# Kernel tuning notes

Measured on AMD Instinct MI355X. Metric: run time of the kernel, lower is better.

The kernel has to match this reference:

```python
import jax, jax.numpy as jnp
import numpy as np

N_TOKENS, DIM = 4096, 2048
N_EXPERTS, TOPK, INTER = 32, 4, 1408
ALPHA, LIMIT, LIN_OFFSET = 1.702, 7.0, 1.0


def quick_geglu(h, probs):
    # h: [..., 2*INTER], interleaved gate/up as in the torch code (x[..., ::2], x[..., 1::2])
    gate = jnp.minimum(h[..., ::2], LIMIT)
    up = jnp.clip(h[..., 1::2], -LIMIT, LIMIT)
    glu = gate * jax.nn.sigmoid(ALPHA * gate)
    return glu * (up + LIN_OFFSET) * probs


def setup_inputs() -> dict:
    key = jax.random.key(0)
    k1, k2, k3, k4, k5 = jax.random.split(key, 5)
    x = jax.random.normal(k1, (N_TOKENS, DIM), dtype=jnp.float32)
    token_mask = jnp.ones((N_TOKENS,), dtype=bool)
    w = jax.random.uniform(k2, (N_TOKENS, TOPK), dtype=jnp.float32)
    weights = w / jnp.sum(w, axis=-1, keepdims=True)  # routing probs
    indices = jax.random.randint(k3, (N_TOKENS, TOPK), 0, N_EXPERTS, dtype=jnp.int64)
    gate_and_up_projs = 0.02 * jax.random.normal(k4, (N_EXPERTS, DIM, 2 * INTER), dtype=jnp.float32)
    down_projs = 0.02 * jax.random.normal(k5, (N_EXPERTS, INTER, DIM), dtype=jnp.float32)
    return {"x": x, "token_mask": token_mask, "weights": weights, "indices": indices,
            "gate_and_up_projs": gate_and_up_projs, "down_projs": down_projs}


def _moe_forward(x, weights, gup, down, token_mask, indices):
    N, D = x.shape
    E = gup.shape[0]
    topk = indices.shape[1]
    T = N * topk
    C = 2 * ((T + E - 1) // E)

    # masked tokens get expert id -1 (as in _permute_tokens_for_grouped_mm)
    flat_e = jnp.where(token_mask[:, None], indices, -1).reshape(-1)
    valid = flat_e >= 0
    e_id = jnp.where(valid, flat_e, E).astype(jnp.int32)  # invalid -> overflow group E
    w = jnp.where(valid, weights.reshape(-1).astype(jnp.float32), 0.0)
    tok = jnp.repeat(jnp.arange(N, dtype=jnp.int32), topk)

    # stable sort by expert (permutation step)
    order = jnp.argsort(e_id)
    se, st, sw = e_id[order], tok[order], w[order]

    # rank of each sorted assignment within its expert group
    counts = jnp.bincount(e_id, length=E + 1)
    starts = jnp.concatenate([jnp.zeros((1,), jnp.int32), jnp.cumsum(counts).astype(jnp.int32)])
    rank = jnp.arange(T, dtype=jnp.int32) - starts[se]
    valid_slot = (se < E) & (rank < C)
    dest = jnp.where(valid_slot, se * C + rank, E * C)  # overflow/dump row E*C

    # scatter permuted tokens into padded per-expert buffers [E, C, D]
    xb = jnp.zeros((E * C + 1, D), x.dtype).at[dest].set(x[st])
    pb = jnp.zeros((E * C + 1,), jnp.float32).at[dest].set(sw)
    tb = jnp.full((E * C + 1,), N, jnp.int32).at[dest].set(st)

    xg = xb[:E * C].reshape(E, C, D)
    h = jnp.einsum('ecd,edh->ech', xg, gup)                       # grouped gate+up GEMM
    a = quick_geglu(h, pb[:E * C].reshape(E, C, 1)).astype(x.dtype)  # fused act * probs
    y = jnp.einsum('ech,ehd->ecd', a, down).reshape(E * C, D)      # grouped down GEMM

    # combine: scatter-add back to token positions (empty slots have prob 0 -> y == 0)
    out = jnp.zeros((N + 1, D), x.dtype).at[tb[:E * C]].add(y)
    return out[:N]


def reference(x, token_mask, weights, indices, gate_and_up_projs, down_projs):
    return _moe_forward(x, weights, gate_and_up_projs, down_projs, token_mask, indices)
```

## Files before the change

kernel.cpp:

```cpp
#include <hip/hip_runtime.h>
#include <hip/hip_bf16.h>
#include <cstdint>
#include <cstddef>

#define N_TOKENS  4096
#define DIM       2048
#define N_EXPERTS 32
#define TOPK      4
#define INTER     1408
#define TWO_INTER 2816
#define CAP       1024
#define T_ASSIGN  (N_TOKENS*TOPK)
#define BK        32

typedef __attribute__((ext_vector_type(8))) short short8;
typedef __attribute__((ext_vector_type(4))) float f32x4;

__device__ __forceinline__ unsigned pack_bf16(float a, float b) {
  unsigned ua = __builtin_bit_cast(unsigned, a);
  unsigned ub = __builtin_bit_cast(unsigned, b);
  ua = (ua + 0x8000u) >> 16;
  ub = (ub + 0x8000u) & 0xFFFF0000u;
  return ua | ub;
}
__device__ __forceinline__ unsigned short bf16_1(float a) {
  return (unsigned short)((__builtin_bit_cast(unsigned, a) + 0x8000u) >> 16);
}
__device__ __forceinline__ float bf2f(unsigned u16) {
  return __builtin_bit_cast(float, u16 << 16);
}

__device__ __forceinline__ void gl_lds16(const void* g, void* l) {
  __builtin_amdgcn_global_load_lds(
      (const __attribute__((address_space(1))) unsigned int*)g,
      (__attribute__((address_space(3))) unsigned int*)l, 16, 0, 0);
}

__global__ void k_build(const int* __restrict__ tmask, const float* __restrict__ w,
                        const int* __restrict__ idx, int* __restrict__ counts,
                        int* __restrict__ tok, float* __restrict__ pb,
                        int* __restrict__ pos) {
  int i = blockIdx.x * 256 + threadIdx.x;
  if (i >= T_ASSIGN) return;
  int t = i >> 2;
  int e = idx[i];
  if (e < 0 || e >= N_EXPERTS) return;
  if (tmask[t] == 0) return;
  int r = atomicAdd(&counts[e], 1);
  if (r < CAP) {
    tok[e * CAP + r] = t;
    pb[e * CAP + r] = w[i];
    pos[i] = e * CAP + r;
  }
}

__global__ __launch_bounds__(256) void k_conv(const float* __restrict__ src,
                                              __hip_bfloat16* __restrict__ dst, int n4) {
  int i = blockIdx.x * 256 + threadIdx.x;
  int stride = gridDim.x * 256;
  for (; i < n4; i += stride) {
    float4 v = *(const float4*)(src + (size_t)i * 4);
    *(uint2*)(dst + (size_t)i * 4) = make_uint2(pack_bf16(v.x, v.y), pack_bf16(v.z, v.w));
  }
}

__global__ __launch_bounds__(256) void k_tconv(const float* __restrict__ src,
                                               __hip_bfloat16* __restrict__ dst,
                                               int R, int C) {
  __shared__ unsigned short s[64][88];
  int nrt = R >> 6, nct = C >> 6;
  int bid = blockIdx.x;
  int e  = bid / (nrt * nct);
  int rr = bid % (nrt * nct);
  int rt = rr / nct, ct = rr % nct;
  int r0 = rt * 64, c0 = ct * 64;
  const float* sp = src + (size_t)e * R * C;
  int t = threadIdx.x;
  int lr  = t >> 4;
  int lc4 = (t & 15) * 4;
  #pragma unroll
  for (int p = 0; p < 4; ++p) {
    int r = lr + p * 16;
    float4 v = *(const float4*)(sp + (size_t)(r0 + r) * C + c0 + lc4);
    s[lc4 + 0][r] = bf16_1(v.x);
    s[lc4 + 1][r] = bf16_1(v.y);
    s[lc4 + 2][r] = bf16_1(v.z);
    s[lc4 + 3][r] = bf16_1(v.w);
  }
  __syncthreads();
  __hip_bfloat16* dp = dst + (size_t)e * C * R;
  int wc   = t >> 2;
  int wr16 = (t & 3) * 16;
  uint4 o0 = *(const uint4*)&s[wc][wr16];
  uint4 o1 = *(const uint4*)&s[wc][wr16 + 8];
  __hip_bfloat16* o = dp + (size_t)(c0 + wc) * R + r0 + wr16;
  *(uint4*)o = o0;
  *(uint4*)(o + 8) = o1;
}

__global__ __launch_bounds__(256) void k_combine(const __hip_bfloat16* __restrict__ y,
                                                 const int* __restrict__ pos,
                                                 float* __restrict__ out) {
  int gid = blockIdx.x * 256 + threadIdx.x;
  int t  = gid >> 8;
  int c8 = (gid & 255) * 8;
  int4 p = *(const int4*)(pos + t * 4);
  float s[8] = {0.f, 0.f, 0.f, 0.f, 0.f, 0.f, 0.f, 0.f};
  #pragma unroll
  for (int k = 0; k < 4; ++k) {
    int pp = (k == 0) ? p.x : (k == 1) ? p.y : (k == 2) ? p.z : p.w;
    if (pp >= 0) {
      uint4 v = *(const uint4*)(y + (size_t)pp * DIM + c8);
      s[0] += bf2f(v.x & 0xffffu); s[1] += bf2f(v.x >> 16);
      s[2] += bf2f(v.y & 0xffffu); s[3] += bf2f(v.y >> 16);
      s[4] += bf2f(v.z & 0xffffu); s[5] += bf2f(v.z >> 16);
      s[6] += bf2f(v.w & 0xffffu); s[7] += bf2f(v.w >> 16);
    }
  }
  float* o = out + (size_t)t * DIM + c8;
  *(float4*)o       = make_float4(s[0], s[1], s[2], s[3]);
  *(float4*)(o + 4) = make_float4(s[4], s[5], s[6], s[7]);
}


#define STGX(tt, KT) do {                                              \
    if ((tt) < (KT)) {                                                 \
      const int k0_ = (tt) * BK;                                       \
      char* base_ = smem + ((tt) & 1) * 24576;                         \
      gl_lds16(aR0 + k0_, base_ + w * 2048 + lane * 16);               \
      gl_lds16(aR1 + k0_, base_ + w * 2048 + 1024 + lane * 16);        \
      gl_lds16(bR  + k0_, base_ + 16384 + w * 1024 + lane * 16);       \
    }                                                                  \
  } while (0)

#define KLOOP(KT) do {                                                 \
    STGX(0, KT);                                                       \
    _Pragma("unroll 1")                                                \
    for (int t = 0; t < (KT); ++t) {                                   \
      STGX(t + 1, KT);                                                 \
      if (t + 1 < (KT)) { asm volatile("s_waitcnt vmcnt(3)" ::: "memory"); } \
      else             { asm volatile("s_waitcnt vmcnt(0)" ::: "memory"); } \
      __builtin_amdgcn_s_barrier();                                    \
      const char* Ab_ = smem + (t & 1) * 24576;                        \
      const char* Bb_ = Ab_ + 16384;                                   \
      short8 af_[4], bf_[4];                                           \
      _Pragma("unroll")                                                \
      for (int mi_ = 0; mi_ < 4; ++mi_)                                \
        af_[mi_] = *(const short8*)(Ab_ + (wr * 64 + mi_ * 16 + (lane & 15)) * 64 + rch); \
      _Pragma("unroll")                                                \
      for (int ni_ = 0; ni_ < 4; ++ni_)                                \
        bf_[ni_] = *(const short8*)(Bb_ + (wc * 64 + ni_ * 16 + (lane & 15)) * 64 + rch); \
      __builtin_amdgcn_s_setprio(1);                                   \
      _Pragma("unroll")                                                \
      for (int mi_ = 0; mi_ < 4; ++mi_)                                \
        _Pragma("unroll")                                              \
        for (int ni_ = 0; ni_ < 4; ++ni_)                              \
          acc[mi_][ni_] = __builtin_amdgcn_mfma_f32_16x16x32_bf16(     \
              af_[mi_], bf_[ni_], acc[mi_][ni_], 0, 0, 0);             \
      __builtin_amdgcn_s_setprio(0);                                   \
      __builtin_amdgcn_s_barrier();                                    \
    }                                                                  \
  } while (0)

__global__ __launch_bounds__(512, 4) void k_gemm1p(
    const __hip_bfloat16* __restrict__ xb, const __hip_bfloat16* __restrict__ gupT,
    const int* __restrict__ counts, const int* __restrict__ tok,
    const float* __restrict__ pb, __hip_bfloat16* __restrict__ act)
{
  __shared__ char smem[49152];
  const int NT = TWO_INTER / 128;
  const int KT = DIM / BK;
  const int xcd  = blockIdx.x & 7;
  const int slot = blockIdx.x >> 3;
  const int tid = threadIdx.x, lane = tid & 63, w = tid >> 6;
  const int wr = w >> 1, wc = w & 1;
  const int csw = ((lane & 3) ^ ((lane >> 3) & 3)) * 8;
  const int rch = (((lane >> 4) ^ ((lane >> 1) & 3)) << 4);
  const int rA0 = w * 32 + (lane >> 2);
  const int rB  = w * 16 + (lane >> 2);

  int k = 0;
  for (int ei = 0; ei < 4; ++ei) {
    const int e = xcd * 4 + ei;
    int cc = counts[e]; cc = cc > CAP ? CAP : cc;
    const int mtc = (cc + 255) >> 8;
    for (int nt = 0; nt < NT; ++nt)
      for (int mt = 0; mt < mtc; ++mt, ++k) {
        if ((k & 63) != slot) continue;
        const int m0 = mt * 256, n0 = nt * 128;
        __syncthreads();

        const __hip_bfloat16* gT = gupT + (size_t)e * TWO_INTER * DIM;
        const __hip_bfloat16* aR0 = xb + (size_t)tok[e * CAP + m0 + rA0] * DIM + csw;
        const __hip_bfloat16* aR1 = xb + (size_t)tok[e * CAP + m0 + rA0 + 16] * DIM + csw;
        const __hip_bfloat16* bR  = gT + (size_t)(n0 + rB) * DIM + csw;

        f32x4 acc[4][4];
        #pragma unroll
        for (int i = 0; i < 4; ++i)
          #pragma unroll
          for (int j = 0; j < 4; ++j) acc[i][j] = (f32x4){0.f, 0.f, 0.f, 0.f};

        KLOOP(KT);

        const int colp = lane & 15;
        const int rgrp = lane >> 4;
        #pragma unroll
        for (int mi = 0; mi < 4; ++mi) {
          #pragma unroll
          for (int j = 0; j < 4; ++j) {
            int rowl = wr * 64 + mi * 16 + rgrp * 4 + j;
            float prob = pb[e * CAP + m0 + rowl];
            size_t arow = (size_t)(e * CAP + m0 + rowl) * INTER;
            #pragma unroll
            for (int ni = 0; ni < 4; ++ni) {
              float v = acc[mi][ni][j];
              float other = __shfl_xor(v, 1, 64);
              if ((lane & 1) == 0) {
                float gate = fminf(v, 7.0f);
                float up   = fminf(fmaxf(other, -7.0f), 7.0f);
                float glu  = gate / (1.0f + __expf(-1.702f * gate));
                float a    = glu * (up + 1.0f) * prob;
                int nh = n0 + wc * 64 + ni * 16 + colp;
                act[arow + (nh >> 1)] = __float2bfloat16(a);
              }
            }
          }
        }
      }
  }
}

__global__ __launch_bounds__(512, 4) void k_gemm2p(
    const __hip_bfloat16* __restrict__ act, const __hip_bfloat16* __restrict__ downT,
    const int* __restrict__ counts, __hip_bfloat16* __restrict__ y)
{
  __shared__ char smem[49152];
  const int NT = DIM / 128;
  const int KT = INTER / BK;
  const int xcd  = blockIdx.x & 7;
  const int slot = blockIdx.x >> 3;
  const int tid = threadIdx.x, lane = tid & 63, w = tid >> 6;
  const int wr = w >> 1, wc = w & 1;
  const int csw = ((lane & 3) ^ ((lane >> 3) & 3)) * 8;
  const int rch = (((lane >> 4) ^ ((lane >> 1) & 3)) << 4);
  const int rA0 = w * 32 + (lane >> 2);
  const int rB  = w * 16 + (lane >> 2);

  int k = 0;
  for (int ei = 0; ei < 4; ++ei) {
    const int e = xcd * 4 + ei;
    int cc = counts[e]; cc = cc > CAP ? CAP : cc;
    const int mtc = (cc + 255) >> 8;
    for (int nt = 0; nt < NT; ++nt)
      for (int mt = 0; mt < mtc; ++mt, ++k) {
        if ((k & 63) != slot) continue;
        const int m0 = mt * 256, n0 = nt * 128;
        __syncthreads();

        const __hip_bfloat16* dT = downT + (size_t)e * DIM * INTER;
        const __hip_bfloat16* aR0 = act + (size_t)(e * CAP + m0 + rA0) * INTER + csw;
        const __hip_bfloat16* aR1 = act + (size_t)(e * CAP + m0 + rA0 + 16) * INTER + csw;
        const __hip_bfloat16* bR  = dT + (size_t)(n0 + rB) * INTER + csw;

        f32x4 acc[4][4];
        #pragma unroll
        for (int i = 0; i < 4; ++i)
          #pragma unroll
          for (int j = 0; j < 4; ++j) acc[i][j] = (f32x4){0.f, 0.f, 0.f, 0.f};

        KLOOP(KT);

        const int colp = lane & 15;
        const int rgrp = lane >> 4;
        #pragma unroll
        for (int mi = 0; mi < 4; ++mi) {
          #pragma unroll
          for (int j = 0; j < 4; ++j) {
            int rowl = wr * 64 + mi * 16 + rgrp * 4 + j;
            __hip_bfloat16* yrow = y + (size_t)(e * CAP + m0 + rowl) * DIM + n0;
            #pragma unroll
            for (int ni = 0; ni < 4; ++ni)
              yrow[wc * 64 + ni * 16 + colp] = __float2bfloat16(acc[mi][ni][j]);
          }
        }
      }
  }
}


extern "C" void kernel_launch(void* const* d_in, const int* in_sizes, int n_in,
                              void* d_out, int out_size, void* d_ws, size_t ws_size,
                              hipStream_t stream) {
  const float* x     = (const float*)d_in[0];
  const int*   tmask = (const int*)d_in[1];
  const float* w     = (const float*)d_in[2];
  const int*   idx   = (const int*)d_in[3];
  const float* gup   = (const float*)d_in[4];
  const float* down  = (const float*)d_in[5];
  float* out = (float*)d_out;

  char* ws = (char*)d_ws;
  const size_t off_tok   = 256;
  const size_t off_pb    = off_tok + 131072;
  const size_t off_pos   = off_pb + 131072;
  const size_t off_act   = off_pos + 65536;
  const size_t act_bytes = (size_t)N_EXPERTS * CAP * INTER * 2;
  const size_t off_xb    = off_act + act_bytes;
  const size_t xb_bytes  = (size_t)N_TOKENS * DIM * 2;
  const size_t off_gupT  = off_xb + xb_bytes;
  const size_t gupT_b    = (size_t)N_EXPERTS * TWO_INTER * DIM * 2;
  const size_t off_downT = off_gupT + gupT_b;

  int*   counts = (int*)ws;
  int*   tok    = (int*)(ws + off_tok);
  float* pbuf   = (float*)(ws + off_pb);
  int*   pos    = (int*)(ws + off_pos);
  __hip_bfloat16* act   = (__hip_bfloat16*)(ws + off_act);
  __hip_bfloat16* xb    = (__hip_bfloat16*)(ws + off_xb);
  __hip_bfloat16* gupT  = (__hip_bfloat16*)(ws + off_gupT);
  __hip_bfloat16* downT = (__hip_bfloat16*)(ws + off_downT);
  __hip_bfloat16* y     = (__hip_bfloat16*)(ws + off_gupT);

  hipMemsetAsync(ws, 0, off_pos, stream);
  hipMemsetAsync(ws + off_pos, 0xFF, 65536, stream);
  k_build<<<(T_ASSIGN + 255) / 256, 256, 0, stream>>>(tmask, w, idx, counts, tok, pbuf, pos);

  k_conv<<<2048, 256, 0, stream>>>(x, xb, (N_TOKENS * DIM) / 4);
  k_tconv<<<N_EXPERTS * (DIM / 64) * (TWO_INTER / 64), 256, 0, stream>>>(gup, gupT, DIM, TWO_INTER);
  k_tconv<<<N_EXPERTS * (INTER / 64) * (DIM / 64), 256, 0, stream>>>(down, downT, INTER, DIM);

  k_gemm1p<<<512, 512, 0, stream>>>(xb, gupT, counts, tok, pbuf, act);
  k_gemm2p<<<512, 512, 0, stream>>>(act, downT, counts, y);
  k_combine<<<N_TOKENS, 256, 0, stream>>>(y, pos, out);
}
```

Measured before the change: 878.5 us.

## Read fp32 weights directly in GEMMs and use atomic work queues per XCD

Drops the two transpose-and-convert kernels that turned the expert weights into bf16 transposed copies. The GEMMs now load fp32 weight tiles straight into a larger LDS buffer and convert them to bf16 while building the MFMA B fragments, using strided scalar LDS reads. Static round-robin tile assignment is replaced by a per-XCD atomic counter work queue. This avoids a full extra read and write of the weights, but doubles the B bytes loaded per tile, adds LDS read and conversion ALU work in the inner loop, and raises LDS use per block.

```diff
diff --git a/kernel.cpp b/kernel.cpp
--- a/kernel.cpp
+++ b/kernel.cpp
@@ -62,40 +62,6 @@
     float4 v = *(const float4*)(src + (size_t)i * 4);
     *(uint2*)(dst + (size_t)i * 4) = make_uint2(pack_bf16(v.x, v.y), pack_bf16(v.z, v.w));
   }
-}
-
-__global__ __launch_bounds__(256) void k_tconv(const float* __restrict__ src,
-                                               __hip_bfloat16* __restrict__ dst,
-                                               int R, int C) {
-  __shared__ unsigned short s[64][88];
-  int nrt = R >> 6, nct = C >> 6;
-  int bid = blockIdx.x;
-  int e  = bid / (nrt * nct);
-  int rr = bid % (nrt * nct);
-  int rt = rr / nct, ct = rr % nct;
-  int r0 = rt * 64, c0 = ct * 64;
-  const float* sp = src + (size_t)e * R * C;
-  int t = threadIdx.x;
-  int lr  = t >> 4;
-  int lc4 = (t & 15) * 4;
-  #pragma unroll
-  for (int p = 0; p < 4; ++p) {
-    int r = lr + p * 16;
-    float4 v = *(const float4*)(sp + (size_t)(r0 + r) * C + c0 + lc4);
-    s[lc4 + 0][r] = bf16_1(v.x);
-    s[lc4 + 1][r] = bf16_1(v.y);
-    s[lc4 + 2][r] = bf16_1(v.z);
-    s[lc4 + 3][r] = bf16_1(v.w);
-  }
-  __syncthreads();
-  __hip_bfloat16* dp = dst + (size_t)e * C * R;
-  int wc   = t >> 2;
-  int wr16 = (t & 3) * 16;
-  uint4 o0 = *(const uint4*)&s[wc][wr16];
-  uint4 o1 = *(const uint4*)&s[wc][wr16 + 8];
-  __hip_bfloat16* o = dp + (size_t)(c0 + wc) * R + r0 + wr16;
-  *(uint4*)o = o0;
-  *(uint4*)(o + 8) = o1;
 }
 
 __global__ __launch_bounds__(256) void k_combine(const __hip_bfloat16* __restrict__ y,
@@ -123,168 +89,204 @@
 }
 
 
-#define STGX(tt, KT) do {                                              \
-    if ((tt) < (KT)) {                                                 \
-      const int k0_ = (tt) * BK;                                       \
-      char* base_ = smem + ((tt) & 1) * 24576;                         \
-      gl_lds16(aR0 + k0_, base_ + w * 2048 + lane * 16);               \
-      gl_lds16(aR1 + k0_, base_ + w * 2048 + 1024 + lane * 16);        \
-      gl_lds16(bR  + k0_, base_ + 16384 + w * 1024 + lane * 16);       \
-    }                                                                  \
+#define STG(tt, KT) do {                                                     \
+    if ((tt) < (KT)) {                                                       \
+      char* base_ = smem + ((tt) & 1) * 32768;                               \
+      const int ka_ = (tt) * BK;                                             \
+      gl_lds16(aR0 + ka_, base_ + w * 2048 + lane * 16);                     \
+      gl_lds16(aR1 + ka_, base_ + w * 2048 + 1024 + lane * 16);              \
+      const size_t kb_ = (size_t)(tt) * BK * LDB;                            \
+      gl_lds16(bR0 + kb_, base_ + 16384 + w * 1024 + lane * 16);             \
+      gl_lds16(bR1 + kb_, base_ + 16384 + 8192 + w * 1024 + lane * 16);      \
+    }                                                                        \
   } while (0)
 
-#define KLOOP(KT) do {                                                 \
-    STGX(0, KT);                                                       \
-    _Pragma("unroll 1")                                                \
-    for (int t = 0; t < (KT); ++t) {                                   \
-      STGX(t + 1, KT);                                                 \
-      if (t + 1 < (KT)) { asm volatile("s_waitcnt vmcnt(3)" ::: "memory"); } \
-      else             { asm volatile("s_waitcnt vmcnt(0)" ::: "memory"); } \
-      __builtin_amdgcn_s_barrier();                                    \
-      const char* Ab_ = smem + (t & 1) * 24576;                        \
-      const char* Bb_ = Ab_ + 16384;                                   \
-      short8 af_[4], bf_[4];                                           \
-      _Pragma("unroll")                                                \
-      for (int mi_ = 0; mi_ < 4; ++mi_)                                \
+#define KLOOP(KT) do {                                                       \
+    STG(0, KT);                                                              \
+    _Pragma("unroll 1")                                                      \
+    for (int t = 0; t < (KT); ++t) {                                         \
+      STG(t + 1, KT);                                                        \
+      if (t + 1 < (KT)) { asm volatile("s_waitcnt vmcnt(4)" ::: "memory"); } \
+      else             { asm volatile("s_waitcnt vmcnt(0)" ::: "memory"); }  \
+      __builtin_amdgcn_s_barrier();                                          \
+      const char* Ab_ = smem + (t & 1) * 32768;                              \
+      const float* bq_ = (const float*)(Ab_ + 16384 + ((lane >> 4) << 3) * 512) \
+                         + (wc * 64 + (lane & 15));                          \
+      short8 af_[4];                                                         \
+      _Pragma("unroll")                                                      \
+      for (int mi_ = 0; mi_ < 4; ++mi_)                                      \
         af_[mi_] = *(const short8*)(Ab_ + (wr * 64 + mi_ * 16 + (lane & 15)) * 64 + rch); \
-      _Pragma("unroll")                                                \
-      for (int ni_ = 0; ni_ < 4; ++ni_)                                \
-        bf_[ni_] = *(const short8*)(Bb_ + (wc * 64 + ni_ * 16 + (lane & 15)) * 64 + rch); \
-      __builtin_amdgcn_s_setprio(1);                                   \
-      _Pragma("unroll")                                                \
-      for (int mi_ = 0; mi_ < 4; ++mi_)                                \
-        _Pragma("unroll")                                              \
-        for (int ni_ = 0; ni_ < 4; ++ni_)                              \
-          acc[mi_][ni_] = __builtin_amdgcn_mfma_f32_16x16x32_bf16(     \
-              af_[mi_], bf_[ni_], acc[mi_][ni_], 0, 0, 0);             \
-      __builtin_amdgcn_s_setprio(0);                                   \
-      __builtin_amdgcn_s_barrier();                                    \
-    }                                                                  \
+      _Pragma("unroll")                                                      \
+      for (int ni_ = 0; ni_ < 4; ++ni_) {                                    \
+        const float* q_ = bq_ + ni_ * 16;                                    \
+        short8 bf_;                                                          \
+        _Pragma("unroll")                                                    \
+        for (int j_ = 0; j_ < 8; ++j_)                                       \
+          bf_[j_] = (short)bf16_1(q_[j_ * 128]);                             \
+        __builtin_amdgcn_s_setprio(1);                                       \
+        _Pragma("unroll")                                                    \
+        for (int mi_ = 0; mi_ < 4; ++mi_)                                    \
+          acc[mi_][ni_] = __builtin_amdgcn_mfma_f32_16x16x32_bf16(           \
+              af_[mi_], bf_, acc[mi_][ni_], 0, 0, 0);                        \
+        __builtin_amdgcn_s_setprio(0);                                       \
+      }                                                                      \
+      __builtin_amdgcn_s_barrier();                                          \
+    }                                                                        \
   } while (0)
 
 __global__ __launch_bounds__(512, 4) void k_gemm1p(
-    const __hip_bfloat16* __restrict__ xb, const __hip_bfloat16* __restrict__ gupT,
+    const __hip_bfloat16* __restrict__ xb, const float* __restrict__ gup,
     const int* __restrict__ counts, const int* __restrict__ tok,
-    const float* __restrict__ pb, __hip_bfloat16* __restrict__ act)
+    const float* __restrict__ pb, __hip_bfloat16* __restrict__ act,
+    int* __restrict__ qh)
 {
-  __shared__ char smem[49152];
+  __shared__ char smem[65536];
+  __shared__ int s_item;
   const int NT = TWO_INTER / 128;
   const int KT = DIM / BK;
-  const int xcd  = blockIdx.x & 7;
-  const int slot = blockIdx.x >> 3;
+  const size_t LDB = TWO_INTER;
+  const int xcd = blockIdx.x & 7;
   const int tid = threadIdx.x, lane = tid & 63, w = tid >> 6;
   const int wr = w >> 1, wc = w & 1;
   const int csw = ((lane & 3) ^ ((lane >> 3) & 3)) * 8;
   const int rch = (((lane >> 4) ^ ((lane >> 1) & 3)) << 4);
   const int rA0 = w * 32 + (lane >> 2);
-  const int rB  = w * 16 + (lane >> 2);
-
-  int k = 0;
+  const int bk0 = tid >> 5;
+  const int bn4 = (tid & 31) * 4;
+
+  int mtcs[4], pre[5];
+  pre[0] = 0;
+  #pragma unroll
   for (int ei = 0; ei < 4; ++ei) {
+    int cc = counts[xcd * 4 + ei]; cc = cc > CAP ? CAP : cc;
+    mtcs[ei] = (cc + 255) >> 8;
+    pre[ei + 1] = pre[ei] + NT * mtcs[ei];
+  }
+  const int total = pre[4];
+
+  for (;;) {
+    if (tid == 0) s_item = atomicAdd(&qh[xcd], 1);
+    __syncthreads();
+    const int it = s_item;
+    if (it >= total) break;
+    int ei = (it >= pre[1]) + (it >= pre[2]) + (it >= pre[3]);
+    int loc = it - pre[ei];
+    int mtc = mtcs[ei];
+    int nt = loc / mtc, mt = loc - nt * mtc;
     const int e = xcd * 4 + ei;
-    int cc = counts[e]; cc = cc > CAP ? CAP : cc;
-    const int mtc = (cc + 255) >> 8;
-    for (int nt = 0; nt < NT; ++nt)
-      for (int mt = 0; mt < mtc; ++mt, ++k) {
-        if ((k & 63) != slot) continue;
-        const int m0 = mt * 256, n0 = nt * 128;
-        __syncthreads();
-
-        const __hip_bfloat16* gT = gupT + (size_t)e * TWO_INTER * DIM;
-        const __hip_bfloat16* aR0 = xb + (size_t)tok[e * CAP + m0 + rA0] * DIM + csw;
-        const __hip_bfloat16* aR1 = xb + (size_t)tok[e * CAP + m0 + rA0 + 16] * DIM + csw;
-        const __hip_bfloat16* bR  = gT + (size_t)(n0 + rB) * DIM + csw;
-
-        f32x4 acc[4][4];
+    const int m0 = mt * 256, n0 = nt * 128;
+
+    const float* gW = gup + (size_t)e * DIM * TWO_INTER + n0;
+    const __hip_bfloat16* aR0 = xb + (size_t)tok[e * CAP + m0 + rA0] * DIM + csw;
+    const __hip_bfloat16* aR1 = xb + (size_t)tok[e * CAP + m0 + rA0 + 16] * DIM + csw;
+    const float* bR0 = gW + (size_t)bk0 * LDB + bn4;
+    const float* bR1 = gW + (size_t)(bk0 + 16) * LDB + bn4;
+
+    f32x4 acc[4][4];
+    #pragma unroll
+    for (int i = 0; i < 4; ++i)
+      #pragma unroll
+      for (int j = 0; j < 4; ++j) acc[i][j] = (f32x4){0.f, 0.f, 0.f, 0.f};
+
+    KLOOP(KT);
+
+    const int colp = lane & 15;
+    const int rgrp = lane >> 4;
+    #pragma unroll
+    for (int mi = 0; mi < 4; ++mi) {
+      #pragma unroll
+      for (int j = 0; j < 4; ++j) {
+        int rowl = wr * 64 + mi * 16 + rgrp * 4 + j;
+        float prob = pb[e * CAP + m0 + rowl];
+        size_t arow = (size_t)(e * CAP + m0 + rowl) * INTER;
         #pragma unroll
-        for (int i = 0; i < 4; ++i)
-          #pragma unroll
-          for (int j = 0; j < 4; ++j) acc[i][j] = (f32x4){0.f, 0.f, 0.f, 0.f};
-
-        KLOOP(KT);
-
-        const int colp = lane & 15;
-        const int rgrp = lane >> 4;
-        #pragma unroll
-        for (int mi = 0; mi < 4; ++mi) {
-          #pragma unroll
-          for (int j = 0; j < 4; ++j) {
-            int rowl = wr * 64 + mi * 16 + rgrp * 4 + j;
-            float prob = pb[e * CAP + m0 + rowl];
-            size_t arow = (size_t)(e * CAP + m0 + rowl) * INTER;
-            #pragma unroll
-            for (int ni = 0; ni < 4; ++ni) {
-              float v = acc[mi][ni][j];
-              float other = __shfl_xor(v, 1, 64);
-              if ((lane & 1) == 0) {
-                float gate = fminf(v, 7.0f);
-                float up   = fminf(fmaxf(other, -7.0f), 7.0f);
-                float glu  = gate / (1.0f + __expf(-1.702f * gate));
-                float a    = glu * (up + 1.0f) * prob;
-                int nh = n0 + wc * 64 + ni * 16 + colp;
-                act[arow + (nh >> 1)] = __float2bfloat16(a);
-              }
-            }
+        for (int ni = 0; ni < 4; ++ni) {
+          float v = acc[mi][ni][j];
+          float other = __shfl_xor(v, 1, 64);
+          if ((lane & 1) == 0) {
+            float gate = fminf(v, 7.0f);
+            float up   = fminf(fmaxf(other, -7.0f), 7.0f);
+            float glu  = gate / (1.0f + __expf(-1.702f * gate));
+            float a    = glu * (up + 1.0f) * prob;
+            int nh = n0 + wc * 64 + ni * 16 + colp;
+            act[arow + (nh >> 1)] = __float2bfloat16(a);
           }
         }
       }
+    }
+    __syncthreads();
   }
 }
 
 __global__ __launch_bounds__(512, 4) void k_gemm2p(
-    const __hip_bfloat16* __restrict__ act, const __hip_bfloat16* __restrict__ downT,
-    const int* __restrict__ counts, __hip_bfloat16* __restrict__ y)
+    const __hip_bfloat16* __restrict__ act, const float* __restrict__ down,
+    const int* __restrict__ counts, __hip_bfloat16* __restrict__ y,
+    int* __restrict__ qh)
 {
-  __shared__ char smem[49152];
+  __shared__ char smem[65536];
+  __shared__ int s_item;
   const int NT = DIM / 128;
   const int KT = INTER / BK;
-  const int xcd  = blockIdx.x & 7;
-  const int slot = blockIdx.x >> 3;
+  const size_t LDB = DIM;
+  const int xcd = blockIdx.x & 7;
   const int tid = threadIdx.x, lane = tid & 63, w = tid >> 6;
   const int wr = w >> 1, wc = w & 1;
   const int csw = ((lane & 3) ^ ((lane >> 3) & 3)) * 8;
   const int rch = (((lane >> 4) ^ ((lane >> 1) & 3)) << 4);
   const int rA0 = w * 32 + (lane >> 2);
-  const int rB  = w * 16 + (lane >> 2);
-
-  int k = 0;
+  const int bk0 = tid >> 5;
+  const int bn4 = (tid & 31) * 4;
+
+  int mtcs[4], pre[5];
+  pre[0] = 0;
+  #pragma unroll
   for (int ei = 0; ei < 4; ++ei) {
+    int cc = counts[xcd * 4 + ei]; cc = cc > CAP ? CAP : cc;
+    mtcs[ei] = (cc + 255) >> 8;
+    pre[ei + 1] = pre[ei] + NT * mtcs[ei];
+  }
+  const int total = pre[4];
+
+  for (;;) {
+    if (tid == 0) s_item = atomicAdd(&qh[xcd], 1);
+    __syncthreads();
+    const int it = s_item;
+    if (it >= total) break;
+    int ei = (it >= pre[1]) + (it >= pre[2]) + (it >= pre[3]);
+    int loc = it - pre[ei];
+    int mtc = mtcs[ei];
+    int nt = loc / mtc, mt = loc - nt * mtc;
     const int e = xcd * 4 + ei;
-    int cc = counts[e]; cc = cc > CAP ? CAP : cc;
-    const int mtc = (cc + 255) >> 8;
-    for (int nt = 0; nt < NT; ++nt)
-      for (int mt = 0; mt < mtc; ++mt, ++k) {
-        if ((k & 63) != slot) continue;
-        const int m0 = mt * 256, n0 = nt * 128;
-        __syncthreads();
-
-        const __hip_bfloat16* dT = downT + (size_t)e * DIM * INTER;
-        const __hip_bfloat16* aR0 = act + (size_t)(e * CAP + m0 + rA0) * INTER + csw;
-        const __hip_bfloat16* aR1 = act + (size_t)(e * CAP + m0 + rA0 + 16) * INTER + csw;
-        const __hip_bfloat16* bR  = dT + (size_t)(n0 + rB) * INTER + csw;
-
-        f32x4 acc[4][4];
+    const int m0 = mt * 256, n0 = nt * 128;
+
+    const float* dW = down + (size_t)e * INTER * DIM + n0;
+    const __hip_bfloat16* aR0 = act + (size_t)(e * CAP + m0 + rA0) * INTER + csw;
+    const __hip_bfloat16* aR1 = act + (size_t)(e * CAP + m0 + rA0 + 16) * INTER + csw;
+    const float* bR0 = dW + (size_t)bk0 * LDB + bn4;
+    const float* bR1 = dW + (size_t)(bk0 + 16) * LDB + bn4;
+
+    f32x4 acc[4][4];
+    #pragma unroll
+    for (int i = 0; i < 4; ++i)
+      #pragma unroll
+      for (int j = 0; j < 4; ++j) acc[i][j] = (f32x4){0.f, 0.f, 0.f, 0.f};
+
+    KLOOP(KT);
+
+    const int colp = lane & 15;
+    const int rgrp = lane >> 4;
+    #pragma unroll
+    for (int mi = 0; mi < 4; ++mi) {
+      #pragma unroll
+      for (int j = 0; j < 4; ++j) {
+        int rowl = wr * 64 + mi * 16 + rgrp * 4 + j;
+        __hip_bfloat16* yrow = y + (size_t)(e * CAP + m0 + rowl) * DIM + n0;
         #pragma unroll
-        for (int i = 0; i < 4; ++i)
-          #pragma unroll
-          for (int j = 0; j < 4; ++j) acc[i][j] = (f32x4){0.f, 0.f, 0.f, 0.f};
-
-        KLOOP(KT);
-
-        const int colp = lane & 15;
-        const int rgrp = lane >> 4;
-        #pragma unroll
-        for (int mi = 0; mi < 4; ++mi) {
-          #pragma unroll
-          for (int j = 0; j < 4; ++j) {
-            int rowl = wr * 64 + mi * 16 + rgrp * 4 + j;
-            __hip_bfloat16* yrow = y + (size_t)(e * CAP + m0 + rowl) * DIM + n0;
-            #pragma unroll
-            for (int ni = 0; ni < 4; ++ni)
-              yrow[wc * 64 + ni * 16 + colp] = __float2bfloat16(acc[mi][ni][j]);
-          }
-        }
+        for (int ni = 0; ni < 4; ++ni)
+          yrow[wc * 64 + ni * 16 + colp] = __float2bfloat16(acc[mi][ni][j]);
       }
+    }
+    __syncthreads();
   }
 }
 
@@ -301,6 +303,8 @@
   float* out = (float*)d_out;
 
   char* ws = (char*)d_ws;
+  const size_t off_qh1   = 128;
+  const size_t off_qh2   = 160;
   const size_t off_tok   = 256;
   const size_t off_pb    = off_tok + 131072;
   const size_t off_pos   = off_pb + 131072;
@@ -308,29 +312,25 @@
   const size_t act_bytes = (size_t)N_EXPERTS * CAP * INTER * 2;
   const size_t off_xb    = off_act + act_bytes;
   const size_t xb_bytes  = (size_t)N_TOKENS * DIM * 2;
-  const size_t off_gupT  = off_xb + xb_bytes;
-  const size_t gupT_b    = (size_t)N_EXPERTS * TWO_INTER * DIM * 2;
-  const size_t off_downT = off_gupT + gupT_b;
+  const size_t off_y     = off_xb + xb_bytes;
 
   int*   counts = (int*)ws;
+  int*   qh1    = (int*)(ws + off_qh1);
+  int*   qh2    = (int*)(ws + off_qh2);
   int*   tok    = (int*)(ws + off_tok);
   float* pbuf   = (float*)(ws + off_pb);
   int*   pos    = (int*)(ws + off_pos);
-  __hip_bfloat16* act   = (__hip_bfloat16*)(ws + off_act);
-  __hip_bfloat16* xb    = (__hip_bfloat16*)(ws + off_xb);
-  __hip_bfloat16* gupT  = (__hip_bfloat16*)(ws + off_gupT);
-  __hip_bfloat16* downT = (__hip_bfloat16*)(ws + off_downT);
-  __hip_bfloat16* y     = (__hip_bfloat16*)(ws + off_gupT);
+  __hip_bfloat16* act = (__hip_bfloat16*)(ws + off_act);
+  __hip_bfloat16* xb  = (__hip_bfloat16*)(ws + off_xb);
+  __hip_bfloat16* y   = (__hip_bfloat16*)(ws + off_y);
 
   hipMemsetAsync(ws, 0, off_pos, stream);
   hipMemsetAsync(ws + off_pos, 0xFF, 65536, stream);
   k_build<<<(T_ASSIGN + 255) / 256, 256, 0, stream>>>(tmask, w, idx, counts, tok, pbuf, pos);
 
   k_conv<<<2048, 256, 0, stream>>>(x, xb, (N_TOKENS * DIM) / 4);
-  k_tconv<<<N_EXPERTS * (DIM / 64) * (TWO_INTER / 64), 256, 0, stream>>>(gup, gupT, DIM, TWO_INTER);
-  k_tconv<<<N_EXPERTS * (INTER / 64) * (DIM / 64), 256, 0, stream>>>(down, downT, INTER, DIM);
-
-  k_gemm1p<<<512, 512, 0, stream>>>(xb, gupT, counts, tok, pbuf, act);
-  k_gemm2p<<<512, 512, 0, stream>>>(act, downT, counts, y);
+
+  k_gemm1p<<<512, 512, 0, stream>>>(xb, gup, counts, tok, pbuf, act, qh1);
+  k_gemm2p<<<512, 512, 0, stream>>>(act, down, counts, y, qh2);
   k_combine<<<N_TOKENS, 256, 0, stream>>>(y, pos, out);
 }
```

After: 802.5 us. -8.6%, faster.
